# Optimization experiments

Measured on AMD Instinct MI355X. Metric: run time of the kernel, lower is better.

Reference implementation:

```python
import jax, jax.numpy as jnp
import numpy as np

ALPHA = 0.2  # LeakyReLU negative slope
NEG_INF = -9e15


def setup_inputs() -> dict:
    key = jax.random.key(0)
    k1, k2, k3, k4 = jax.random.split(key, 4)
    B, N, Fin, Fout = 4, 4096, 256, 128
    h = jax.random.normal(k1, (B, N, Fin), dtype=jnp.float32)
    adj = jax.random.randint(k2, (B, N, N), 0, 2, dtype=jnp.int32)  # {0,1} adjacency
    # xavier_uniform with gain 1.414
    limW = 1.414 * np.sqrt(6.0 / (Fin + Fout))
    W = jax.random.uniform(k3, (Fin, Fout), jnp.float32, -limW, limW)
    lima = 1.414 * np.sqrt(6.0 / (2 * Fout + 1))
    a = jax.random.uniform(k4, (2 * Fout, 1), jnp.float32, -lima, lima)
    return {"h": h, "adj": adj, "W": W, "a": a}


def reference(h, adj, W, a):
    # Wh: [B, N, Fout]
    Wh = jnp.einsum('bni,io->bno', h, W)
    Fout = W.shape[1]
    # Decompose a^T [Wh_i || Wh_j] = a1.Wh_i + a2.Wh_j (identical math, avoids
    # materializing the [B,N,N,2F] concat tensor the torch code builds).
    a1, a2 = a[:Fout, 0], a[Fout:, 0]
    s1 = jnp.einsum('bno,o->bn', Wh, a1)  # [B, N]
    s2 = jnp.einsum('bno,o->bn', Wh, a2)  # [B, N]
    e = jax.nn.leaky_relu(s1[:, :, None] + s2[:, None, :], negative_slope=ALPHA)  # [B,N,N]
    attention = jnp.where(adj > 0, e, jnp.asarray(NEG_INF, e.dtype))
    attention = jax.nn.softmax(attention, axis=2)
    # dropout is inactive in eval mode (training=False)
    # Faithful to the torch code: the FIRST h_prime is overwritten; the output is
    # einsum('bjk,bji->bki', attention, Wh) -> sums over the softmax (row) axis j.
    h_prime = jnp.einsum('bjk,bji->bki', attention, Wh)  # [B, N, Fout]
    return jax.nn.elu(h_prime)  # concat=True
```

## Files before the change

### kernel.cpp

```cpp
#include <hip/hip_runtime.h>
#include <hip/hip_bf16.h>

#define ALPHA 0.2f
#define L2E 1.4426950408889634f

constexpr int Nn = 4096;
constexpr int FIN = 256;
constexpr int FOUT = 128;
constexpr int JC = 8;
constexpr int JQ = 512;
constexpr int NCH = 16;
constexpr long long SLAB = 2097152;

typedef __attribute__((ext_vector_type(8))) short short8;
typedef __attribute__((ext_vector_type(8))) unsigned short ushort8;
typedef __attribute__((ext_vector_type(4))) float f32x4;
typedef __attribute__((ext_vector_type(16))) float f32x16;
typedef __attribute__((ext_vector_type(4))) int int4v;

__device__ __forceinline__ unsigned short f2bf(float x) {
  unsigned int u = __float_as_uint(x);
  unsigned int r = (u + 0x7fffu + ((u >> 16) & 1u)) >> 16;
  return (unsigned short)r;
}

__device__ __forceinline__ void gload16(const void* g, void* l) {
  auto lp = (__attribute__((address_space(3))) void*)l;
  auto gp = (const __attribute__((address_space(1))) void*)g;
  __builtin_amdgcn_global_load_lds(gp, lp, 16, 0, 0);
}

__global__ __launch_bounds__(256) void k0_prep(
    const float* __restrict__ W, const float* __restrict__ a,
    unsigned short* __restrict__ WT, float* __restrict__ wa) {
  int t = threadIdx.x;
  int blk = blockIdx.x;
  if (blk < 8) {
    __shared__ float lw[32][132];
    int kc0 = blk * 32;
#pragma unroll
    for (int m = 0; m < 4; ++m) {
      int idx = t * 16 + m * 4;
      f32x4 v = *(const f32x4*)(W + kc0 * 128 + idx);
      int k = idx >> 7, i0 = idx & 127;
      *(f32x4*)&lw[k][i0] = v;
    }
    __syncthreads();
    int i = t >> 1, half = t & 1;
    unsigned short pk[16];
#pragma unroll
    for (int kk = 0; kk < 16; ++kk) pk[kk] = f2bf(lw[half * 16 + kk][i]);
    ushort8* dst = (ushort8*)(WT + i * 256 + kc0 + half * 16);
    dst[0] = *(ushort8*)&pk[0];
    dst[1] = *(ushort8*)&pk[8];
  } else {
    float acc1 = 0.f, acc2 = 0.f;
    const float* Wr = W + t * 128;
#pragma unroll
    for (int m = 0; m < 32; ++m) {
      f32x4 wv = *(const f32x4*)(Wr + m * 4);
      f32x4 a1 = *(const f32x4*)(a + m * 4);
      f32x4 a2 = *(const f32x4*)(a + 128 + m * 4);
      acc1 += wv.x * a1.x + wv.y * a1.y + wv.z * a1.z + wv.w * a1.w;
      acc2 += wv.x * a2.x + wv.y * a2.y + wv.z * a2.z + wv.w * a2.w;
    }
    wa[t] = acc1;
    wa[256 + t] = acc2;
  }
}

__global__ __launch_bounds__(256) void k1a_scores(
    const float* __restrict__ h, const float* __restrict__ wa,
    float* __restrict__ s1L, float* __restrict__ s2L) {
  int t = threadIdx.x;
  int wv = t >> 6, l = t & 63;
  int row = blockIdx.x * 4 + wv;
  f32x4 hv = *(const f32x4*)(h + (long long)row * 256 + l * 4);
  f32x4 w1 = ((const f32x4*)wa)[l];
  f32x4 w2 = ((const f32x4*)wa)[64 + l];
  float v1 = hv.x * w1.x + hv.y * w1.y + hv.z * w1.z + hv.w * w1.w;
  float v2 = hv.x * w2.x + hv.y * w2.y + hv.z * w2.z + hv.w * w2.w;
#pragma unroll
  for (int off = 32; off; off >>= 1) {
    v1 += __shfl_xor(v1, off);
    v2 += __shfl_xor(v2, off);
  }
  if (l == 0) {
    s1L[row] = v1 * L2E;
    s2L[row] = v2 * L2E;
  }
}

__global__ __launch_bounds__(256) void k1b_wh(
    const float* __restrict__ h, const unsigned short* __restrict__ WT,
    unsigned short* __restrict__ whT) {
  __shared__ __align__(16) char smem[49152];
  int t = threadIdx.x;
  int w = t >> 6, l = t & 63, g = l >> 4, r = l & 15;
  int r0 = blockIdx.x * 64;
  int b = r0 >> 12, nbase = r0 & 4095;

  f32x4 acc[8];
#pragma unroll
  for (int s = 0; s < 8; ++s) acc[s] = (f32x4){0.f, 0.f, 0.f, 0.f};

  for (int kc = 0; kc < 2; ++kc) {
    __syncthreads();
    {
      int row = t >> 2, q4 = t & 3;
      const f32x4* src =
          (const f32x4*)(h + (long long)(r0 + row) * 256 + kc * 128 + q4 * 32);
#pragma unroll
      for (int m = 0; m < 4; ++m) {
        f32x4 v0 = src[m * 2], v1 = src[m * 2 + 1];
        unsigned int pk[4];
        pk[0] = ((unsigned)f2bf(v0.y) << 16) | f2bf(v0.x);
        pk[1] = ((unsigned)f2bf(v0.w) << 16) | f2bf(v0.z);
        pk[2] = ((unsigned)f2bf(v1.y) << 16) | f2bf(v1.x);
        pk[3] = ((unsigned)f2bf(v1.w) << 16) | f2bf(v1.z);
        int slot = q4 * 4 + m;
        *(ushort8*)(smem + row * 256 + ((slot ^ (row & 7)) << 4)) =
            *(ushort8*)pk;
      }
    }
    {
      int i = t >> 1, pt = t & 1;
      const ushort8* src = (const ushort8*)(WT + i * 256 + kc * 128 + pt * 64);
#pragma unroll
      for (int m = 0; m < 8; ++m) {
        ushort8 v = src[m];
        int slot = pt * 8 + m;
        *(ushort8*)(smem + 16384 + i * 256 + ((slot ^ (i & 7)) << 4)) = v;
      }
    }
    __syncthreads();
#pragma unroll
    for (int kk = 0; kk < 4; ++kk) {
      int arow = w * 16 + r;
      short8 af = *(const short8*)(smem + arow * 256 +
                                   (((kk * 4 + g) ^ (arow & 7)) << 4));
#pragma unroll
      for (int s = 0; s < 8; ++s) {
        int i = s * 16 + r;
        short8 bf = *(const short8*)(smem + 16384 + i * 256 +
                                     (((kk * 4 + g) ^ (i & 7)) << 4));
        acc[s] =
            __builtin_amdgcn_mfma_f32_16x16x32_bf16(af, bf, acc[s], 0, 0, 0);
      }
    }
  }

  __syncthreads();
  unsigned short* tb = (unsigned short*)smem;
#pragma unroll
  for (int s = 0; s < 8; ++s)
#pragma unroll
    for (int q = 0; q < 4; ++q)
      tb[(s * 16 + r) * 72 + w * 16 + 4 * g + q] = f2bf(acc[s][q]);
  __syncthreads();
  {
    int i = t >> 1, half = t & 1;
    const ushort8* src = (const ushort8*)(tb + i * 72 + half * 32);
    ushort8* dst = (ushort8*)(whT + (((long long)(b * 128 + i)) << 12) + nbase +
                              half * 32);
#pragma unroll
    for (int m = 0; m < 4; ++m) dst[m] = src[m];
  }
}

__global__ __launch_bounds__(256) void k2_stats(
    const int* __restrict__ adj, const float* __restrict__ s1L,
    const float* __restrict__ s2L, float2* __restrict__ st2,
    unsigned long long* __restrict__ mask64) {
  __shared__ unsigned int mwords[128];
  __shared__ float wsum[4];
  int row = blockIdx.x;
  int b = row >> 12;
  int t = threadIdx.x;
  float s1j = s1L[row];
  const int4v* arow = (const int4v*)(adj + (long long)row * Nn);
  const f32x4* s2v = (const f32x4*)(s2L + (b << 12));

  float sum = 0.f;
#pragma unroll
  for (int q = 0; q < 4; ++q) {
    int4v av = arow[q * 256 + t];
    f32x4 sv = s2v[q * 256 + t];
    unsigned nib = 0;
#pragma unroll
    for (int c = 0; c < 4; ++c) {
      float u = s1j + sv[c];
      float vL = fmaxf(u, ALPHA * u);
      float e = exp2f(vL);
      sum += (av[c] > 0) ? e : 0.f;
      nib |= ((unsigned)(av[c] > 0)) << c;
    }
    unsigned n1 = nib | (__shfl_xor(nib, 1) << 4);
    unsigned n2 = n1 | (__shfl_xor(n1, 2) << 8);
    unsigned n4 = n2 | (__shfl_xor(n2, 4) << 16);
    if ((t & 7) == 0) mwords[q * 32 + (t >> 3)] = n4;
  }
#pragma unroll
  for (int off = 32; off; off >>= 1) sum += __shfl_xor(sum, off);
  if ((t & 63) == 0) wsum[t >> 6] = sum;
  __syncthreads();
  if (t < 64) {
    unsigned long long mv = *(unsigned long long*)&mwords[t * 2];
    mask64[((long long)row << 6) + t] = mv;
  }
  if (t == 0) {
    float S = wsum[0] + wsum[1] + wsum[2] + wsum[3];
    float negc = (S > 0.f) ? -log2f(S) : -1.0e30f;
    st2[row] = make_float2(s1j, negc);
  }
}

__global__ __launch_bounds__(512, 4) void k3_pv(
    const unsigned short* __restrict__ whT, const float2* __restrict__ st2,
    const unsigned long long* __restrict__ mask64,
    const float* __restrict__ s2L, unsigned short* __restrict__ pbuf) {
  __shared__ __align__(16) char smem[36864];
  char* mbase = smem + 16384;
  float2* stl = (float2*)(smem + 32768);

  int t = threadIdx.x;
  int orig = blockIdx.x;
  int swz = (orig & 7) * 64 + (orig >> 3);
  int kt = swz & 15, jc = (swz >> 4) & 7, b = swz >> 7;
  int w = t >> 6, l = t & 63, hl = l >> 5, ln = l & 31;
  int jq0 = jc * JQ;
  long long brow = (long long)(b << 12);
  int k0 = kt << 8;
  float s2k = s2L[brow + k0 + w * 32 + ln];

  if (t < 256) gload16(st2 + brow + jq0 + t * 2, (char*)stl + t * 16);
  {
    const char* msrc =
        (const char*)(mask64 + ((brow + jq0 + t) << 6) + kt * 4);
    gload16(msrc, mbase + t * 16);
    gload16(msrc + 16, mbase + 8192 + t * 16);
  }
  const unsigned short* whTb = whT + ((long long)b << 19);
  int gj = t >> 7, gi = t & 127;
  const unsigned short* wsrc = whTb + (long long)gi * 4096 + jq0 + gj * 8;
  gload16(wsrc, smem + t * 16);
  __syncthreads();

  char* mwv = mbase + (w >> 2) * 8192 + (w & 3) * 4;

  f32x16 acc[4];
#pragma unroll
  for (int q = 0; q < 4; ++q)
#pragma unroll
    for (int r = 0; r < 16; ++r) acc[q][r] = 0.f;

  for (int ch = 0; ch < NCH; ++ch) {
    int cur = ch & 1;
    if (ch + 1 < NCH)
      gload16(wsrc + (ch + 1) * 32, smem + (cur ^ 1) * 8192 + t * 16);
    char* wb = smem + cur * 8192;
    int jb = ch * 32 + hl * 8;
#pragma unroll
    for (int s = 0; s < 2; ++s) {
      short8 af;
#pragma unroll
      for (int e = 0; e < 8; ++e) {
        int ja = jb + s * 16 + e;
        float2 sc = stl[ja];
        unsigned int mv = *(unsigned int*)(mwv + ja * 16);
        float u = sc.x + s2k;
        float vL = fmaxf(u, ALPHA * u);
        float p = exp2f(vL + sc.y);
        p = ((mv >> ln) & 1u) ? p : 0.f;
        __hip_bfloat16 hb = __float2bfloat16(p);
        af[e] = *(short*)&hb;
      }
      int gbase = (2 * s + hl) * 2048;
#pragma unroll
      for (int q = 0; q < 4; ++q) {
        short8 bv = *(const short8*)(wb + gbase + ((q * 32 + ln) << 4));
        acc[q] =
            __builtin_amdgcn_mfma_f32_32x32x16_bf16(af, bv, acc[q], 0, 0, 0);
      }
    }
    __syncthreads();
  }

  unsigned short* pb = pbuf + (long long)jc * SLAB + ((brow + k0) << 7);
#pragma unroll
  for (int q = 0; q < 4; ++q) {
#pragma unroll
    for (int r = 0; r < 16; ++r) {
      int kl = (r & 3) + ((r >> 2) << 3) + (hl << 2) + (w << 5);
      pb[kl * 128 + q * 32 + ln] = f2bf(acc[q][r]);
    }
  }
}

__global__ __launch_bounds__(256) void k4_reduce(
    const unsigned short* __restrict__ pbuf, float* __restrict__ out) {
  int base = (blockIdx.x * 256 + threadIdx.x) * 8;
  float s[8] = {0.f, 0.f, 0.f, 0.f, 0.f, 0.f, 0.f, 0.f};
#pragma unroll
  for (int sl = 0; sl < JC; ++sl) {
    ushort8 v = *(const ushort8*)(pbuf + (long long)sl * SLAB + base);
#pragma unroll
    for (int e = 0; e < 8; ++e)
      s[e] += __uint_as_float(((unsigned)(unsigned short)v[e]) << 16);
  }
  f32x4 o0, o1;
#pragma unroll
  for (int e = 0; e < 8; ++e) {
    float x = s[e];
    float y = x > 0.f ? x : expm1f(x);
    if (e < 4) o0[e] = y; else o1[e - 4] = y;
  }
  *(f32x4*)(out + base) = o0;
  *(f32x4*)(out + base + 4) = o1;
}

extern "C" void kernel_launch(void* const* d_in, const int* in_sizes, int n_in,
                              void* d_out, int out_size, void* d_ws,
                              size_t ws_size, hipStream_t stream) {
  const float* h = (const float*)d_in[0];
  const int* adj = (const int*)d_in[1];
  const float* W = (const float*)d_in[2];
  const float* a = (const float*)d_in[3];
  float* out = (float*)d_out;

  char* ws = (char*)d_ws;
  unsigned short* WT = (unsigned short*)ws;
  float* wa = (float*)(ws + 65536);
  unsigned short* whT = (unsigned short*)(ws + (1 << 20));
  float* s1L = (float*)(ws + (5 << 20));
  float* s2L = s1L + 16384;
  float2* st2 = (float2*)(ws + (5 << 20) + (128 << 10));
  unsigned long long* mask64 =
      (unsigned long long*)(ws + (6 << 20));
  unsigned short* pbuf = (unsigned short*)(ws + (16 << 20));

  hipLaunchKernelGGL(k0_prep, dim3(9), dim3(256), 0, stream, W, a, WT, wa);
  hipLaunchKernelGGL(k1a_scores, dim3(4096), dim3(256), 0, stream, h, wa, s1L,
                     s2L);
  hipLaunchKernelGGL(k1b_wh, dim3(256), dim3(256), 0, stream, h, WT, whT);
  hipLaunchKernelGGL(k2_stats, dim3(16384), dim3(256), 0, stream, adj, s1L,
                     s2L, st2, mask64);
  hipLaunchKernelGGL(k3_pv, dim3(512), dim3(512), 0, stream, whT, st2, mask64,
                     s2L, pbuf);
  hipLaunchKernelGGL(k4_reduce, dim3(1024), dim3(256), 0, stream, pbuf, out);
}
```

Before: 128.8 us.

## Fuse score computation into Wh GEMM, precombine leaky-relu terms, add nontemporal accesses

Removes the separate score kernel and the W·a precompute. s1/s2 are now computed from the bf16 Wh tile inside the Wh GEMM kernel, which is retiled to 16 rows per block over 1024 blocks. The stats kernel stores s1+negc and alpha*s1+negc, so the PV kernel evaluates exp2(max(e1,e2)) with fewer ops per element. Nontemporal loads and stores are added for adj and the partial buffers. Scores now come from bf16-rounded Wh instead of fp32, which slightly changes numerics, and it saves one launch plus a full extra read of h.

Result: faster. 122.3 us (-5.0%).

```diff
diff --git a/kernel.cpp b/kernel.cpp
--- a/kernel.cpp
+++ b/kernel.cpp
@@ -24,6 +24,10 @@
   return (unsigned short)r;
 }
 
+__device__ __forceinline__ float bf2f(unsigned short v) {
+  return __uint_as_float(((unsigned)v) << 16);
+}
+
 __device__ __forceinline__ void gload16(const void* g, void* l) {
   auto lp = (__attribute__((address_space(3))) void*)l;
   auto gp = (const __attribute__((address_space(1))) void*)g;
@@ -31,97 +35,54 @@
 }
 
 __global__ __launch_bounds__(256) void k0_prep(
-    const float* __restrict__ W, const float* __restrict__ a,
-    unsigned short* __restrict__ WT, float* __restrict__ wa) {
+    const float* __restrict__ W, unsigned short* __restrict__ WT) {
+  __shared__ float lw[32][132];
   int t = threadIdx.x;
-  int blk = blockIdx.x;
-  if (blk < 8) {
-    __shared__ float lw[32][132];
-    int kc0 = blk * 32;
-#pragma unroll
-    for (int m = 0; m < 4; ++m) {
-      int idx = t * 16 + m * 4;
-      f32x4 v = *(const f32x4*)(W + kc0 * 128 + idx);
-      int k = idx >> 7, i0 = idx & 127;
-      *(f32x4*)&lw[k][i0] = v;
-    }
-    __syncthreads();
-    int i = t >> 1, half = t & 1;
-    unsigned short pk[16];
-#pragma unroll
-    for (int kk = 0; kk < 16; ++kk) pk[kk] = f2bf(lw[half * 16 + kk][i]);
-    ushort8* dst = (ushort8*)(WT + i * 256 + kc0 + half * 16);
-    dst[0] = *(ushort8*)&pk[0];
-    dst[1] = *(ushort8*)&pk[8];
-  } else {
-    float acc1 = 0.f, acc2 = 0.f;
-    const float* Wr = W + t * 128;
-#pragma unroll
-    for (int m = 0; m < 32; ++m) {
-      f32x4 wv = *(const f32x4*)(Wr + m * 4);
-      f32x4 a1 = *(const f32x4*)(a + m * 4);
-      f32x4 a2 = *(const f32x4*)(a + 128 + m * 4);
-      acc1 += wv.x * a1.x + wv.y * a1.y + wv.z * a1.z + wv.w * a1.w;
-      acc2 += wv.x * a2.x + wv.y * a2.y + wv.z * a2.z + wv.w * a2.w;
-    }
-    wa[t] = acc1;
-    wa[256 + t] = acc2;
-  }
-}
-
-__global__ __launch_bounds__(256) void k1a_scores(
-    const float* __restrict__ h, const float* __restrict__ wa,
-    float* __restrict__ s1L, float* __restrict__ s2L) {
-  int t = threadIdx.x;
-  int wv = t >> 6, l = t & 63;
-  int row = blockIdx.x * 4 + wv;
-  f32x4 hv = *(const f32x4*)(h + (long long)row * 256 + l * 4);
-  f32x4 w1 = ((const f32x4*)wa)[l];
-  f32x4 w2 = ((const f32x4*)wa)[64 + l];
-  float v1 = hv.x * w1.x + hv.y * w1.y + hv.z * w1.z + hv.w * w1.w;
-  float v2 = hv.x * w2.x + hv.y * w2.y + hv.z * w2.z + hv.w * w2.w;
-#pragma unroll
-  for (int off = 32; off; off >>= 1) {
-    v1 += __shfl_xor(v1, off);
-    v2 += __shfl_xor(v2, off);
-  }
-  if (l == 0) {
-    s1L[row] = v1 * L2E;
-    s2L[row] = v2 * L2E;
-  }
+  int kc0 = blockIdx.x * 32;
+#pragma unroll
+  for (int m = 0; m < 4; ++m) {
+    int idx = t * 16 + m * 4;
+    f32x4 v = *(const f32x4*)(W + kc0 * 128 + idx);
+    int k = idx >> 7, i0 = idx & 127;
+    *(f32x4*)&lw[k][i0] = v;
+  }
+  __syncthreads();
+  int i = t >> 1, half = t & 1;
+  unsigned short pk[16];
+#pragma unroll
+  for (int kk = 0; kk < 16; ++kk) pk[kk] = f2bf(lw[half * 16 + kk][i]);
+  ushort8* dst = (ushort8*)(WT + i * 256 + kc0 + half * 16);
+  dst[0] = *(ushort8*)&pk[0];
+  dst[1] = *(ushort8*)&pk[8];
 }
 
 __global__ __launch_bounds__(256) void k1b_wh(
     const float* __restrict__ h, const unsigned short* __restrict__ WT,
-    unsigned short* __restrict__ whT) {
-  __shared__ __align__(16) char smem[49152];
+    const float* __restrict__ a, unsigned short* __restrict__ whT,
+    float* __restrict__ s1L, float* __restrict__ s2L) {
+  __shared__ __align__(16) char smem[36864];
   int t = threadIdx.x;
   int w = t >> 6, l = t & 63, g = l >> 4, r = l & 15;
-  int r0 = blockIdx.x * 64;
+  int r0 = blockIdx.x * 16;
   int b = r0 >> 12, nbase = r0 & 4095;
 
-  f32x4 acc[8];
-#pragma unroll
-  for (int s = 0; s < 8; ++s) acc[s] = (f32x4){0.f, 0.f, 0.f, 0.f};
+  f32x4 acc[2];
+  acc[0] = (f32x4){0.f, 0.f, 0.f, 0.f};
+  acc[1] = (f32x4){0.f, 0.f, 0.f, 0.f};
 
   for (int kc = 0; kc < 2; ++kc) {
     __syncthreads();
     {
-      int row = t >> 2, q4 = t & 3;
+      int row = t >> 4, sec = t & 15;
       const f32x4* src =
-          (const f32x4*)(h + (long long)(r0 + row) * 256 + kc * 128 + q4 * 32);
-#pragma unroll
-      for (int m = 0; m < 4; ++m) {
-        f32x4 v0 = src[m * 2], v1 = src[m * 2 + 1];
-        unsigned int pk[4];
-        pk[0] = ((unsigned)f2bf(v0.y) << 16) | f2bf(v0.x);
-        pk[1] = ((unsigned)f2bf(v0.w) << 16) | f2bf(v0.z);
-        pk[2] = ((unsigned)f2bf(v1.y) << 16) | f2bf(v1.x);
-        pk[3] = ((unsigned)f2bf(v1.w) << 16) | f2bf(v1.z);
-        int slot = q4 * 4 + m;
-        *(ushort8*)(smem + row * 256 + ((slot ^ (row & 7)) << 4)) =
-            *(ushort8*)pk;
-      }
+          (const f32x4*)(h + (long long)(r0 + row) * 256 + kc * 128 + sec * 8);
+      f32x4 v0 = src[0], v1 = src[1];
+      unsigned int pk[4];
+      pk[0] = ((unsigned)f2bf(v0.y) << 16) | f2bf(v0.x);
+      pk[1] = ((unsigned)f2bf(v0.w) << 16) | f2bf(v0.z);
+      pk[2] = ((unsigned)f2bf(v1.y) << 16) | f2bf(v1.x);
+      pk[3] = ((unsigned)f2bf(v1.w) << 16) | f2bf(v1.z);
+      *(ushort8*)(smem + row * 256 + ((sec ^ (row & 7)) << 4)) = *(ushort8*)pk;
     }
     {
       int i = t >> 1, pt = t & 1;
@@ -130,19 +91,18 @@
       for (int m = 0; m < 8; ++m) {
         ushort8 v = src[m];
         int slot = pt * 8 + m;
-        *(ushort8*)(smem + 16384 + i * 256 + ((slot ^ (i & 7)) << 4)) = v;
+        *(ushort8*)(smem + 4096 + i * 256 + ((slot ^ (i & 7)) << 4)) = v;
       }
     }
     __syncthreads();
 #pragma unroll
     for (int kk = 0; kk < 4; ++kk) {
-      int arow = w * 16 + r;
-      short8 af = *(const short8*)(smem + arow * 256 +
-                                   (((kk * 4 + g) ^ (arow & 7)) << 4));
-#pragma unroll
-      for (int s = 0; s < 8; ++s) {
-        int i = s * 16 + r;
-        short8 bf = *(const short8*)(smem + 16384 + i * 256 +
+      short8 af =
+          *(const short8*)(smem + r * 256 + (((kk * 4 + g) ^ (r & 7)) << 4));
+#pragma unroll
+      for (int s = 0; s < 2; ++s) {
+        int i = w * 32 + s * 16 + r;
+        short8 bf = *(const short8*)(smem + 4096 + i * 256 +
                                      (((kk * 4 + g) ^ (i & 7)) << 4));
         acc[s] =
             __builtin_amdgcn_mfma_f32_16x16x32_bf16(af, bf, acc[s], 0, 0, 0);
@@ -153,18 +113,42 @@
   __syncthreads();
   unsigned short* tb = (unsigned short*)smem;
 #pragma unroll
-  for (int s = 0; s < 8; ++s)
+  for (int s = 0; s < 2; ++s)
 #pragma unroll
     for (int q = 0; q < 4; ++q)
-      tb[(s * 16 + r) * 72 + w * 16 + 4 * g + q] = f2bf(acc[s][q]);
-  __syncthreads();
+      tb[(w * 32 + s * 16 + r) * 24 + g * 4 + q] = f2bf(acc[s][q]);
+  __syncthreads();
+
   {
     int i = t >> 1, half = t & 1;
-    const ushort8* src = (const ushort8*)(tb + i * 72 + half * 32);
-    ushort8* dst = (ushort8*)(whT + (((long long)(b * 128 + i)) << 12) + nbase +
-                              half * 32);
-#pragma unroll
-    for (int m = 0; m < 4; ++m) dst[m] = src[m];
+    ushort8 v = *(const ushort8*)(tb + i * 24 + half * 8);
+    *(ushort8*)(whT + (((long long)(b * 128 + i)) << 12) + nbase + half * 8) =
+        v;
+  }
+  {
+    int n = t >> 4, seg = t & 15;
+    f32x4 a10 = *(const f32x4*)(a + seg * 8);
+    f32x4 a11 = *(const f32x4*)(a + seg * 8 + 4);
+    f32x4 a20 = *(const f32x4*)(a + 128 + seg * 8);
+    f32x4 a21 = *(const f32x4*)(a + 128 + seg * 8 + 4);
+    float v1 = 0.f, v2 = 0.f;
+#pragma unroll
+    for (int m = 0; m < 8; ++m) {
+      float wh = bf2f(tb[(seg * 8 + m) * 24 + n]);
+      float c1 = (m < 4) ? a10[m] : a11[m - 4];
+      float c2 = (m < 4) ? a20[m] : a21[m - 4];
+      v1 += wh * c1;
+      v2 += wh * c2;
+    }
+#pragma unroll
+    for (int off = 8; off; off >>= 1) {
+      v1 += __shfl_xor(v1, off);
+      v2 += __shfl_xor(v2, off);
+    }
+    if (seg == 0) {
+      s1L[r0 + n] = v1 * L2E;
+      s2L[r0 + n] = v2 * L2E;
+    }
   }
 }
 
@@ -184,7 +168,7 @@
   float sum = 0.f;
 #pragma unroll
   for (int q = 0; q < 4; ++q) {
-    int4v av = arow[q * 256 + t];
+    int4v av = __builtin_nontemporal_load(arow + q * 256 + t);
     f32x4 sv = s2v[q * 256 + t];
     unsigned nib = 0;
 #pragma unroll
@@ -211,7 +195,7 @@
   if (t == 0) {
     float S = wsum[0] + wsum[1] + wsum[2] + wsum[3];
     float negc = (S > 0.f) ? -log2f(S) : -1.0e30f;
-    st2[row] = make_float2(s1j, negc);
+    st2[row] = make_float2(s1j + negc, ALPHA * s1j + negc);
   }
 }
 
@@ -231,12 +215,12 @@
   int jq0 = jc * JQ;
   long long brow = (long long)(b << 12);
   int k0 = kt << 8;
-  float s2k = s2L[brow + k0 + w * 32 + ln];
+  float z1 = s2L[brow + k0 + w * 32 + ln];
+  float z2 = ALPHA * z1;
 
   if (t < 256) gload16(st2 + brow + jq0 + t * 2, (char*)stl + t * 16);
   {
-    const char* msrc =
-        (const char*)(mask64 + ((brow + jq0 + t) << 6) + kt * 4);
+    const char* msrc = (const char*)(mask64 + ((brow + jq0 + t) << 6) + kt * 4);
     gload16(msrc, mbase + t * 16);
     gload16(msrc + 16, mbase + 8192 + t * 16);
   }
@@ -268,9 +252,9 @@
         int ja = jb + s * 16 + e;
         float2 sc = stl[ja];
         unsigned int mv = *(unsigned int*)(mwv + ja * 16);
-        float u = sc.x + s2k;
-        float vL = fmaxf(u, ALPHA * u);
-        float p = exp2f(vL + sc.y);
+        float e1 = sc.x + z1;
+        float e2 = sc.y + z2;
+        float p = exp2f(fmaxf(e1, e2));
         p = ((mv >> ln) & 1u) ? p : 0.f;
         __hip_bfloat16 hb = __float2bfloat16(p);
         af[e] = *(short*)&hb;
@@ -292,7 +276,8 @@
 #pragma unroll
     for (int r = 0; r < 16; ++r) {
       int kl = (r & 3) + ((r >> 2) << 3) + (hl << 2) + (w << 5);
-      pb[kl * 128 + q * 32 + ln] = f2bf(acc[q][r]);
+      __builtin_nontemporal_store(f2bf(acc[q][r]),
+                                  pb + kl * 128 + q * 32 + ln);
     }
   }
 }
@@ -303,7 +288,8 @@
   float s[8] = {0.f, 0.f, 0.f, 0.f, 0.f, 0.f, 0.f, 0.f};
 #pragma unroll
   for (int sl = 0; sl < JC; ++sl) {
-    ushort8 v = *(const ushort8*)(pbuf + (long long)sl * SLAB + base);
+    ushort8 v = __builtin_nontemporal_load(
+        (const ushort8*)(pbuf + (long long)sl * SLAB + base));
 #pragma unroll
     for (int e = 0; e < 8; ++e)
       s[e] += __uint_as_float(((unsigned)(unsigned short)v[e]) << 16);
@@ -330,7 +316,6 @@
 
   char* ws = (char*)d_ws;
   unsigned short* WT = (unsigned short*)ws;
-  float* wa = (float*)(ws + 65536);
   unsigned short* whT = (unsigned short*)(ws + (1 << 20));
   float* s1L = (float*)(ws + (5 << 20));
   float* s2L = s1L + 16384;
@@ -339,10 +324,9 @@
       (unsigned long long*)(ws + (6 << 20));
   unsigned short* pbuf = (unsigned short*)(ws + (16 << 20));
 
-  hipLaunchKernelGGL(k0_prep, dim3(9), dim3(256), 0, stream, W, a, WT, wa);
-  hipLaunchKernelGGL(k1a_scores, dim3(4096), dim3(256), 0, stream, h, wa, s1L,
-                     s2L);
-  hipLaunchKernelGGL(k1b_wh, dim3(256), dim3(256), 0, stream, h, WT, whT);
+  hipLaunchKernelGGL(k0_prep, dim3(8), dim3(256), 0, stream, W, WT);
+  hipLaunchKernelGGL(k1b_wh, dim3(1024), dim3(256), 0, stream, h, WT, a, whT,
+                     s1L, s2L);
   hipLaunchKernelGGL(k2_stats, dim3(16384), dim3(256), 0, stream, adj, s1L,
                      s2L, st2, mask64);
   hipLaunchKernelGGL(k3_pv, dim3(512), dim3(512), 0, stream, whT, st2, mask64,
```
